# Optimization experiments

Measured on AMD Instinct MI355X. Metric: run time of the kernel, lower is better.

Reference implementation:

```python
import jax, jax.numpy as jnp
import numpy as np

SIZE = 2048      # codebook entries
DIM = 64         # code dimension (= channels)
DECAY = 0.99
EPS = 1e-05


def setup_inputs() -> dict:
    key = jax.random.key(0)
    k_in, k_emb, k_avg, k_cs = jax.random.split(key, 4)
    inputs = jax.random.normal(k_in, (32, DIM, 4096), dtype=jnp.float32)
    # kaiming-uniform style init for the codebook (kmeans_init=False path)
    bound = np.sqrt(6.0 / DIM)
    embedding = jax.random.uniform(k_emb, (SIZE, DIM), minval=-bound, maxval=bound, dtype=jnp.float32)
    embedding_avg = embedding.copy()
    # warm cluster sizes (buffer state after some training)
    cluster_size = jax.random.uniform(k_cs, (SIZE,), minval=0.5, maxval=64.0, dtype=jnp.float32)
    return {"inputs": inputs, "embedding": embedding, "embedding_avg": embedding_avg, "cluster_size": cluster_size}


def reference(inputs, embedding, embedding_avg, cluster_size):
    B, C, F = inputs.shape
    # [B, C, F] -> [B*F, C]
    flat = inputs.transpose(0, 2, 1).reshape(-1, C)

    dists = (jnp.sum(flat * flat, axis=1, keepdims=True)
             - 2.0 * (flat @ embedding.T)
             + jnp.sum(embedding * embedding, axis=1))
    idx = jnp.argmin(dists, axis=1)            # [N]
    quant_flat = embedding[idx]                # [N, C] gather

    # EMA update (training path), one-hot scatter expressed as segment sums
    cs_batch = jax.ops.segment_sum(jnp.ones_like(idx, dtype=flat.dtype), idx, num_segments=SIZE)
    emb_sum = jax.ops.segment_sum(flat, idx, num_segments=SIZE)  # [SIZE, C]
    new_cluster_size = DECAY * cluster_size + (1.0 - DECAY) * cs_batch
    new_embedding_avg = DECAY * embedding_avg + (1.0 - DECAY) * emb_sum
    n = jnp.sum(new_cluster_size)
    smoothed = (new_cluster_size + EPS) / (n + SIZE * EPS) * jnp.maximum(n, 1.0)
    new_embedding = new_embedding_avg / smoothed[:, None]

    commitment_loss = jnp.mean(jnp.square(flat - jax.lax.stop_gradient(quant_flat)))

    # straight-through estimator (training mode)
    q_ste = flat + jax.lax.stop_gradient(quant_flat - flat)
    quantized = q_ste.reshape(B, F, C).transpose(0, 2, 1)
    indices = idx.reshape(B, F)
    return quantized, indices, commitment_loss, new_embedding, new_cluster_size, new_embedding_avg
```

## Files before the change

kernel.cpp:

```cpp
#include <hip/hip_runtime.h>
#include <stdint.h>

#define VQSIZE 2048
#define DIM 64
#define BATCH 32
#define FEAT 4096
#define NROWS (BATCH*FEAT)
#define DECAYF 0.99f
#define ONEMD 0.01f
#define EPSF 1e-5f
#define MARGIN 2e-3f
#define RCAP 8192

typedef __attribute__((ext_vector_type(8))) short bf16x8;
typedef __attribute__((ext_vector_type(4))) float f32x4;

#define WS_CS     0
#define WS_EMBSUM 2048
#define WS_LOSS   (WS_EMBSUM + VQSIZE*DIM)
#define WS_RC_I   (WS_LOSS + 1)
#define WS_SMOOTH (WS_LOSS + 2)
#define WS_ENORM  135172
#define WS_EHI_F  137220
#define WS_ELO_F  (WS_EHI_F + 65536)
#define WS_RLIST  (WS_ELO_F + 65536)
#define WS_ZERO_FLOATS (WS_LOSS + 2)

#define OUT_QUANT 0
#define OUT_IDX   (BATCH*DIM*FEAT)
#define OUT_LOSS  (OUT_IDX + NROWS)
#define OUT_NEMB  (OUT_LOSS + 1)
#define OUT_NCS   (OUT_NEMB + VQSIZE*DIM)
#define OUT_NEA   (OUT_NCS + VQSIZE)

__device__ __forceinline__ int swz(int row, int k) {
    return row * 128 + ((((k >> 3) ^ (row & 7))) << 4) + ((k & 7) << 1);
}

__device__ __forceinline__ uint16_t f2bf(float x) {
    uint32_t u = __builtin_bit_cast(uint32_t, x);
    u += 0x7fff + ((u >> 16) & 1);
    return (uint16_t)(u >> 16);
}
__device__ __forceinline__ float bf2f(uint16_t b) {
    return __builtin_bit_cast(float, (uint32_t)b << 16);
}

__device__ __forceinline__ void gload16(const void* g, void* l) {
    __builtin_amdgcn_global_load_lds(
        (const __attribute__((address_space(1))) uint32_t*)g,
        (__attribute__((address_space(3))) uint32_t*)l, 16, 0, 0);
}

__global__ void prep_kernel(const float* __restrict__ emb, float* __restrict__ ws) {
    const int e = blockIdx.x * 256 + threadIdx.x;
    const float* er = emb + (size_t)e * DIM;
    char* ehi = (char*)(ws + WS_EHI_F) + (e >> 7) * 16384;
    char* elo = (char*)(ws + WS_ELO_F) + (e >> 7) * 16384;
    const int erow = e & 127;
    float s = 0.f;
#pragma unroll
    for (int k = 0; k < DIM; k += 2) {
        float x0 = er[k], x1 = er[k + 1];
        s += x0 * x0 + x1 * x1;
        uint16_t h0 = f2bf(x0), h1 = f2bf(x1);
        uint16_t l0 = f2bf(x0 - bf2f(h0)), l1 = f2bf(x1 - bf2f(h1));
        int off = swz(erow, k);
        *(uint32_t*)(ehi + off) = (uint32_t)h0 | ((uint32_t)h1 << 16);
        *(uint32_t*)(elo + off) = (uint32_t)l0 | ((uint32_t)l1 << 16);
    }
    ws[WS_ENORM + e] = s;
}

#define NCHUNK (VQSIZE/128)
#define MFMA(a, b, c) __builtin_amdgcn_mfma_f32_16x16x32_bf16(a, b, c, 0, 0, 0)

__launch_bounds__(256, 2)
__global__ void assign_mfma_kernel(const float* __restrict__ in,
                                   float* __restrict__ ws,
                                   float* __restrict__ out) {
    __shared__ __align__(16) char sXhi[16384];
    __shared__ __align__(16) char sXlo[16384];
    __shared__ __align__(16) char sEhi[16384];
    __shared__ __align__(16) char sElo[16384];
    __shared__ __align__(16) float sNorm[VQSIZE];

    const int t = threadIdx.x;
    const int lane = t & 63;
    const int w = t >> 6;
    const int rbase = blockIdx.x * 128;
    const int b = rbase >> 12;
    const int f0 = rbase & (FEAT - 1);

    {
        const float* base = in + (size_t)b * DIM * FEAT + f0;
#pragma unroll
        for (int i = 0; i < 4; ++i) {
            const int c0 = ((t >> 5) & 7) * 2 + i * 16;
#pragma unroll
            for (int m = 0; m < 4; ++m) {
                const int r = (t & 31) + m * 32;
                float x0 = base[(size_t)c0 * FEAT + r];
                float x1 = base[(size_t)(c0 + 1) * FEAT + r];
                uint16_t h0 = f2bf(x0), h1 = f2bf(x1);
                uint16_t l0 = f2bf(x0 - bf2f(h0)), l1 = f2bf(x1 - bf2f(h1));
                int off = swz(r, c0);
                *(uint32_t*)(sXhi + off) = (uint32_t)h0 | ((uint32_t)h1 << 16);
                *(uint32_t*)(sXlo + off) = (uint32_t)l0 | ((uint32_t)l1 << 16);
            }
        }
    }
    {
        const char* gsrc = (const char*)(ws + WS_ENORM);
#pragma unroll
        for (int q = 0; q < 2; ++q) {
            int off = (w * 2 + q) * 1024;
            gload16(gsrc + off + lane * 16, (char*)sNorm + off);
        }
    }
    __syncthreads();

    bf16x8 xh[2][2], xl[2][2];
    {
        const int rl = w * 32 + (lane & 15);
        const int kb0 = (lane >> 4) * 8;
#pragma unroll
        for (int rt = 0; rt < 2; ++rt)
#pragma unroll
            for (int s = 0; s < 2; ++s) {
                int off = swz(rl + rt * 16, s * 32 + kb0);
                xh[rt][s] = *(const bf16x8*)(sXhi + off);
                xl[rt][s] = *(const bf16x8*)(sXlo + off);
            }
    }

    float best0 = 3.4e38f, best1 = 3.4e38f;
    float sec0  = 3.4e38f, sec1  = 3.4e38f;
    int bidx0 = 0, bidx1 = 0;
    const char* gEhi = (const char*)(ws + WS_EHI_F);
    const char* gElo = (const char*)(ws + WS_ELO_F);
    const int kb = (lane >> 4) * 8;
    const int jbase = (lane >> 4) * 4;

    for (int chunk = 0; chunk < NCHUNK; ++chunk) {
        __syncthreads();
        {
            const char* gh = gEhi + chunk * 16384 + w * 4096 + lane * 16;
            const char* gl = gElo + chunk * 16384 + w * 4096 + lane * 16;
            char* lh = sEhi + w * 4096;
            char* ll = sElo + w * 4096;
#pragma unroll
            for (int q = 0; q < 4; ++q) {
                gload16(gh + q * 1024, lh + q * 1024);
                gload16(gl + q * 1024, ll + q * 1024);
            }
        }
        __syncthreads();

#pragma unroll 2
        for (int et = 0; et < 8; ++et) {
            const int er = et * 16 + (lane & 15);
            bf16x8 eh0 = *(const bf16x8*)(sEhi + swz(er, kb));
            bf16x8 eh1 = *(const bf16x8*)(sEhi + swz(er, 32 + kb));
            bf16x8 el0 = *(const bf16x8*)(sElo + swz(er, kb));
            bf16x8 el1 = *(const bf16x8*)(sElo + swz(er, 32 + kb));
            f32x4 en = *(const f32x4*)(sNorm + chunk * 128 + et * 16 + jbase);

            f32x4 acc0 = {0.f, 0.f, 0.f, 0.f};
            f32x4 acc1 = {0.f, 0.f, 0.f, 0.f};
            acc0 = MFMA(eh0, xh[0][0], acc0);
            acc1 = MFMA(eh0, xh[1][0], acc1);
            acc0 = MFMA(eh1, xh[0][1], acc0);
            acc1 = MFMA(eh1, xh[1][1], acc1);
            acc0 = MFMA(el0, xh[0][0], acc0);
            acc1 = MFMA(el0, xh[1][0], acc1);
            acc0 = MFMA(el1, xh[0][1], acc0);
            acc1 = MFMA(el1, xh[1][1], acc1);
            acc0 = MFMA(eh0, xl[0][0], acc0);
            acc1 = MFMA(eh0, xl[1][0], acc1);
            acc0 = MFMA(eh1, xl[0][1], acc0);
            acc1 = MFMA(eh1, xl[1][1], acc1);

            const int eib = chunk * 128 + et * 16 + jbase;
#pragma unroll
            for (int j = 0; j < 4; ++j) {
                float s0 = fmaf(acc0[j], -2.f, en[j]);
                if (s0 < best0) { sec0 = best0; best0 = s0; bidx0 = eib + j; }
                else            sec0 = fminf(sec0, s0);
                float s1 = fmaf(acc1[j], -2.f, en[j]);
                if (s1 < best1) { sec1 = best1; best1 = s1; bidx1 = eib + j; }
                else            sec1 = fminf(sec1, s1);
            }
        }
    }

#pragma unroll
    for (int off = 16; off <= 32; off <<= 1) {
        float ob = __shfl_xor(best0, off); int oi = __shfl_xor(bidx0, off);
        float os = __shfl_xor(sec0, off);
        bool take = (ob < best0) || (ob == best0 && oi < bidx0);
        sec0 = take ? fminf(best0, os) : fminf(ob, sec0);
        if (take) { best0 = ob; bidx0 = oi; }

        ob = __shfl_xor(best1, off); oi = __shfl_xor(bidx1, off);
        os = __shfl_xor(sec1, off);
        take = (ob < best1) || (ob == best1 && oi < bidx1);
        sec1 = take ? fminf(best1, os) : fminf(ob, sec1);
        if (take) { best1 = ob; bidx1 = oi; }
    }
    if (lane < 16) {
        int* wsi = (int*)ws;
        int row0 = rbase + w * 32 + lane;
        int row1 = row0 + 16;
        out[OUT_IDX + row0] = (float)bidx0;
        out[OUT_IDX + row1] = (float)bidx1;
        if (sec0 - best0 < MARGIN) {
            int slot = atomicAdd(&wsi[WS_RC_I], 1);
            if (slot < RCAP) wsi[WS_RLIST + slot] = row0;
        }
        if (sec1 - best1 < MARGIN) {
            int slot = atomicAdd(&wsi[WS_RC_I], 1);
            if (slot < RCAP) wsi[WS_RLIST + slot] = row1;
        }
    }
}

__launch_bounds__(256)
__global__ void rescue_kernel(const float* __restrict__ in,
                              const float* __restrict__ emb,
                              const float* __restrict__ ws,
                              float* __restrict__ out) {
    __shared__ float sx[8][64];
    __shared__ int   srow[8];
    __shared__ float rs[256];
    __shared__ int   ri[256];
    const int t = threadIdx.x;
    const int* wsi = (const int*)ws;
    int cnt = wsi[WS_RC_I];
    if (cnt > RCAP) cnt = RCAP;

    for (int base = blockIdx.x * 8; base < cnt; base += gridDim.x * 8) {
        int nr = cnt - base; if (nr > 8) nr = 8;
        if (t < 8) srow[t] = (t < nr) ? wsi[WS_RLIST + base + t] : 0;
        __syncthreads();
        {
            int rr = t >> 5;
            int k = (t & 31) * 2;
            if (rr < nr) {
                int row = srow[rr];
                int b = row >> 12, f = row & (FEAT - 1);
                const float* xin = in + (size_t)b * DIM * FEAT + f;
                sx[rr][k]     = xin[(size_t)k * FEAT];
                sx[rr][k + 1] = xin[(size_t)(k + 1) * FEAT];
            }
        }
        __syncthreads();
        for (int rr = 0; rr < nr; ++rr) {
            float bs = 3.4e38f; int bi = 0;
            for (int q = 0; q < 8; ++q) {
                int e = t * 8 + q;
                const float4* ep = (const float4*)(emb + (size_t)e * DIM);
                float acc = 0.f;
#pragma unroll
                for (int k4 = 0; k4 < 16; ++k4) {
                    float4 v = ep[k4];
                    acc += sx[rr][k4*4]*v.x + sx[rr][k4*4+1]*v.y
                         + sx[rr][k4*4+2]*v.z + sx[rr][k4*4+3]*v.w;
                }
                float s = ws[WS_ENORM + e] - 2.f * acc;
                if (s < bs) { bs = s; bi = e; }
            }
            rs[t] = bs; ri[t] = bi;
            __syncthreads();
            for (int off2 = 128; off2; off2 >>= 1) {
                if (t < off2) {
                    float o = rs[t + off2]; int oi2 = ri[t + off2];
                    if (o < rs[t] || (o == rs[t] && oi2 < ri[t])) { rs[t] = o; ri[t] = oi2; }
                }
                __syncthreads();
            }
            if (t == 0) out[OUT_IDX + srow[rr]] = (float)ri[0];
            __syncthreads();
        }
        __syncthreads();
    }
}

__launch_bounds__(256, 2)
__global__ void epilogue_kernel(const float* __restrict__ in,
                                const float* __restrict__ emb,
                                float* __restrict__ out,
                                float* __restrict__ ws) {
    __shared__ float sx[64 * 265];
    __shared__ int   sidx[256];
    __shared__ float lred[4];

    const int t = threadIdx.x;
    const int r = blockIdx.x * 256 + t;
    const int b = r >> 12;
    const int f = r & (FEAT - 1);

    const int idx = (int)out[OUT_IDX + r];
    sidx[t] = idx;
    atomicAdd(&ws[WS_CS + idx], 1.0f);

    const float4* eq = (const float4*)(emb + (size_t)idx * DIM);
    const float* xin = in + (size_t)b * DIM * FEAT + f;
    float* qout = out + (size_t)b * DIM * FEAT + f;
    float lsum = 0.f;
#pragma unroll
    for (int c4 = 0; c4 < 16; ++c4) {
        float4 e4 = eq[c4];
        const float ev[4] = {e4.x, e4.y, e4.z, e4.w};
#pragma unroll
        for (int m = 0; m < 4; ++m) {
            int c = c4 * 4 + m;
            float xv = xin[(size_t)c * FEAT];
            qout[(size_t)c * FEAT] = ev[m];
            float d = xv - ev[m];
            lsum += d * d;
            sx[c * 265 + t] = xv;
        }
    }
#pragma unroll
    for (int off = 32; off; off >>= 1) lsum += __shfl_down(lsum, off, 64);
    if ((t & 63) == 0) lred[t >> 6] = lsum;
    __syncthreads();
    if (t == 0) atomicAdd(&ws[WS_LOSS], lred[0] + lred[1] + lred[2] + lred[3]);

    const int w = t >> 6, lane = t & 63;
    float* es = ws + WS_EMBSUM;
    for (int q = 0; q < 64; ++q) {
        int rr = w * 64 + q;
        atomicAdd(es + (size_t)sidx[rr] * 64 + lane, sx[lane * 265 + rr]);
    }
}

__launch_bounds__(1024)
__global__ void finalize_cs(const float* __restrict__ cs,
                            float* __restrict__ out,
                            float* __restrict__ ws) {
    __shared__ float red[16];
    const int t = threadIdx.x;
    float ncs0 = DECAYF * cs[t]        + ONEMD * ws[WS_CS + t];
    float ncs1 = DECAYF * cs[t + 1024] + ONEMD * ws[WS_CS + t + 1024];
    out[OUT_NCS + t]        = ncs0;
    out[OUT_NCS + t + 1024] = ncs1;

    float s = ncs0 + ncs1;
#pragma unroll
    for (int off = 32; off; off >>= 1) s += __shfl_down(s, off, 64);
    int wid = t >> 6, lane = t & 63;
    if (lane == 0) red[wid] = s;
    __syncthreads();
    if (t < 64) {
        float v = (t < 16) ? red[t] : 0.f;
#pragma unroll
        for (int off = 8; off; off >>= 1) v += __shfl_down(v, off, 64);
        if (t == 0) red[0] = v;
    }
    __syncthreads();
    const float n = red[0];
    const float nmax = fmaxf(n, 1.0f);
    const float inv_denom = 1.0f / (n + (float)VQSIZE * EPSF);
    ws[WS_SMOOTH + t]        = (ncs0 + EPSF) * inv_denom * nmax;
    ws[WS_SMOOTH + t + 1024] = (ncs1 + EPSF) * inv_denom * nmax;
    if (t == 0) out[OUT_LOSS] = ws[WS_LOSS] * (1.0f / ((float)NROWS * (float)DIM));
}

__global__ void finalize_emb(const float* __restrict__ ea,
                             float* __restrict__ out,
                             const float* __restrict__ ws) {
    int i = blockIdx.x * 256 + threadIdx.x;
    int e = i >> 6;
    float nea = DECAYF * ea[i] + ONEMD * ws[WS_EMBSUM + i];
    out[OUT_NEA + i] = nea;
    out[OUT_NEMB + i] = nea / ws[WS_SMOOTH + e];
}

extern "C" void kernel_launch(void* const* d_in, const int* in_sizes, int n_in,
                              void* d_out, int out_size, void* d_ws, size_t ws_size,
                              hipStream_t stream) {
    const float* inputs    = (const float*)d_in[0];
    const float* embedding = (const float*)d_in[1];
    const float* emb_avg   = (const float*)d_in[2];
    const float* cluster   = (const float*)d_in[3];
    float* out = (float*)d_out;
    float* ws  = (float*)d_ws;

    hipMemsetAsync(ws, 0, (size_t)WS_ZERO_FLOATS * sizeof(float), stream);

    prep_kernel<<<VQSIZE / 256, 256, 0, stream>>>(embedding, ws);
    assign_mfma_kernel<<<NROWS / 128, 256, 0, stream>>>(inputs, ws, out);
    rescue_kernel<<<256, 256, 0, stream>>>(inputs, embedding, ws, out);
    epilogue_kernel<<<NROWS / 256, 256, 0, stream>>>(inputs, embedding, out, ws);
    finalize_cs<<<1, 1024, 0, stream>>>(cluster, out, ws);
    finalize_emb<<<VQSIZE * DIM / 256, 256, 0, stream>>>(emb_avg, out, ws);
}
```

Measured before the change: 390.2 us.

## Tighten rescue margin and restructure rescue kernel to one row per wavefront

Shrinks the near-tie margin that sends rows from the bf16 MFMA assignment to the exact fp32 rescue pass, so fewer rows get rechecked. The rescue kernel now gives each 64-lane wavefront its own row: each lane scans 32 codebook entries with four split accumulators, and a shuffle-xor argmin replaces the shared-memory tree reduction and its barriers. A smaller margin risks leaving some near-ties on the bf16 result and so changing indices compared with the exact reference.

New measurement: 338.5 us. -13.3%, faster.

```diff
diff --git a/kernel.cpp b/kernel.cpp
--- a/kernel.cpp
+++ b/kernel.cpp
@@ -9,8 +9,9 @@
 #define DECAYF 0.99f
 #define ONEMD 0.01f
 #define EPSF 1e-5f
-#define MARGIN 2e-3f
+#define MARGIN 5e-4f
 #define RCAP 8192
+#define RGRID 256
 
 typedef __attribute__((ext_vector_type(8))) short bf16x8;
 typedef __attribute__((ext_vector_type(4))) float f32x4;
@@ -230,58 +231,45 @@
                               const float* __restrict__ emb,
                               const float* __restrict__ ws,
                               float* __restrict__ out) {
-    __shared__ float sx[8][64];
-    __shared__ int   srow[8];
-    __shared__ float rs[256];
-    __shared__ int   ri[256];
+    __shared__ float xbuf[4][64];
     const int t = threadIdx.x;
+    const int w = t >> 6, lane = t & 63;
     const int* wsi = (const int*)ws;
     int cnt = wsi[WS_RC_I];
     if (cnt > RCAP) cnt = RCAP;
-
-    for (int base = blockIdx.x * 8; base < cnt; base += gridDim.x * 8) {
-        int nr = cnt - base; if (nr > 8) nr = 8;
-        if (t < 8) srow[t] = (t < nr) ? wsi[WS_RLIST + base + t] : 0;
+    const int nbat = (cnt + 4 * RGRID - 1) / (4 * RGRID);
+
+    for (int it = 0; it < nbat; ++it) {
+        const int i = (it * RGRID + blockIdx.x) * 4 + w;
+        const bool active = i < cnt;
+        const int row = active ? wsi[WS_RLIST + i] : 0;
+        const int b = row >> 12, f = row & (FEAT - 1);
+        xbuf[w][lane] = in[(size_t)b * DIM * FEAT + (size_t)lane * FEAT + f];
         __syncthreads();
-        {
-            int rr = t >> 5;
-            int k = (t & 31) * 2;
-            if (rr < nr) {
-                int row = srow[rr];
-                int b = row >> 12, f = row & (FEAT - 1);
-                const float* xin = in + (size_t)b * DIM * FEAT + f;
-                sx[rr][k]     = xin[(size_t)k * FEAT];
-                sx[rr][k + 1] = xin[(size_t)(k + 1) * FEAT];
-            }
-        }
-        __syncthreads();
-        for (int rr = 0; rr < nr; ++rr) {
-            float bs = 3.4e38f; int bi = 0;
-            for (int q = 0; q < 8; ++q) {
-                int e = t * 8 + q;
-                const float4* ep = (const float4*)(emb + (size_t)e * DIM);
-                float acc = 0.f;
-#pragma unroll
-                for (int k4 = 0; k4 < 16; ++k4) {
-                    float4 v = ep[k4];
-                    acc += sx[rr][k4*4]*v.x + sx[rr][k4*4+1]*v.y
-                         + sx[rr][k4*4+2]*v.z + sx[rr][k4*4+3]*v.w;
-                }
-                float s = ws[WS_ENORM + e] - 2.f * acc;
-                if (s < bs) { bs = s; bi = e; }
-            }
-            rs[t] = bs; ri[t] = bi;
-            __syncthreads();
-            for (int off2 = 128; off2; off2 >>= 1) {
-                if (t < off2) {
-                    float o = rs[t + off2]; int oi2 = ri[t + off2];
-                    if (o < rs[t] || (o == rs[t] && oi2 < ri[t])) { rs[t] = o; ri[t] = oi2; }
-                }
-                __syncthreads();
-            }
-            if (t == 0) out[OUT_IDX + srow[rr]] = (float)ri[0];
-            __syncthreads();
-        }
+
+        float bs = 3.4e38f; int bi = 0;
+        const int e0 = lane * 32;
+        for (int q = 0; q < 32; ++q) {
+            const int e = e0 + q;
+            const float4* ep = (const float4*)(emb + (size_t)e * DIM);
+            float a0 = 0.f, a1 = 0.f, a2 = 0.f, a3 = 0.f;
+#pragma unroll
+            for (int k4 = 0; k4 < 16; ++k4) {
+                float4 v = ep[k4];
+                a0 += xbuf[w][k4*4 + 0] * v.x;
+                a1 += xbuf[w][k4*4 + 1] * v.y;
+                a2 += xbuf[w][k4*4 + 2] * v.z;
+                a3 += xbuf[w][k4*4 + 3] * v.w;
+            }
+            float s = ws[WS_ENORM + e] - 2.f * ((a0 + a1) + (a2 + a3));
+            if (s < bs) { bs = s; bi = e; }
+        }
+#pragma unroll
+        for (int off = 1; off <= 32; off <<= 1) {
+            float ob = __shfl_xor(bs, off); int oi = __shfl_xor(bi, off);
+            if (ob < bs || (ob == bs && oi < bi)) { bs = ob; bi = oi; }
+        }
+        if (active && lane == 0) out[OUT_IDX + row] = (float)bi;
         __syncthreads();
     }
 }
@@ -392,7 +380,7 @@
 
     prep_kernel<<<VQSIZE / 256, 256, 0, stream>>>(embedding, ws);
     assign_mfma_kernel<<<NROWS / 128, 256, 0, stream>>>(inputs, ws, out);
-    rescue_kernel<<<256, 256, 0, stream>>>(inputs, embedding, ws, out);
+    rescue_kernel<<<RGRID, 256, 0, stream>>>(inputs, embedding, ws, out);
     epilogue_kernel<<<NROWS / 256, 256, 0, stream>>>(inputs, embedding, out, ws);
     finalize_cs<<<1, 1024, 0, stream>>>(cluster, out, ws);
     finalize_emb<<<VQSIZE * DIM / 256, 256, 0, stream>>>(emb_avg, out, ws);
```
